# Kernel tuning notes

Measured on AMD Instinct MI355X. Metric: run time of the kernel, lower is better.

## Reference

```python
import jax, jax.numpy as jnp
import numpy as np

B_SZ, L, H, P = 16, 1024, 256, 256
DT_MIN, DT_MAX = 1e-3, 1e-1


def setup_inputs() -> dict:
    key = jax.random.key(0)
    ks = jax.random.split(key, 6)
    u = jax.random.normal(ks[0], (B_SZ, L, H), dtype=jnp.float32)
    # Stable diagonal init (stands in for HiPPO-LegS diag: negative real part,
    # spread imaginary parts) so exp(Lambda*Delta) has |.|<1 over long scans.
    Lambda_re = -0.5 * jnp.ones((P,), jnp.float32)
    Lambda_im = jnp.pi * jnp.arange(P, dtype=jnp.float32)
    Bp = jax.random.normal(ks[1], (P, H, 2), jnp.float32) / jnp.sqrt(2.0 * H)  # (P,H,2) real/imag
    Cp = jax.random.normal(ks[2], (H, P, 2), jnp.float32) / jnp.sqrt(2.0 * P)  # (H,P,2) real/imag
    D = jax.random.normal(ks[3], (H,), jnp.float32)
    log_step = (jax.random.uniform(ks[4], (P, 1), jnp.float32)
                * (jnp.log(DT_MAX) - jnp.log(DT_MIN)) + jnp.log(DT_MIN))
    return {"u": u, "Lambda_re": Lambda_re, "Lambda_im": Lambda_im,
            "B": Bp, "C": Cp, "D": D, "log_step": log_step}


def _binop(ei, ej):
    # S5 associative scan element: (A, Bu); compose linear recurrences.
    ai, bi = ei
    aj, bj = ej
    return aj * ai, aj * bi + bj


def reference(u, Lambda_re, Lambda_im, B, C, D, log_step):
    # clip_eigs=False, step_rescale=1.0, conj_sym=True, discretization='zoh'
    Lambda = Lambda_re + 1j * Lambda_im                     # (P,) complex
    B_tilde = B[..., 0] + 1j * B[..., 1]                    # (P,H) complex
    C_tilde = C[..., 0] + 1j * C[..., 1]                    # (H,P) complex
    Delta = jnp.exp(log_step[:, 0])                         # (P,)
    # ZOH discretization
    Lambda_bar = jnp.exp(Lambda * Delta)                    # (P,)
    B_bar = ((Lambda_bar - 1.0) / Lambda)[:, None] * B_tilde  # (P,H)
    # Input projection: (B, L, P) complex
    Bu = jnp.einsum('ph,blh->blp', B_bar, u.astype(B_bar.dtype))
    Lam = jnp.broadcast_to(Lambda_bar, Bu.shape)            # (B, L, P)
    # Parallel associative scan over time axis
    _, xs = jax.lax.associative_scan(_binop, (Lam, Bu), axis=1)  # states (B,L,P)
    # Output projection; conj_sym -> 2 * real part
    ys = 2.0 * jnp.einsum('hp,blp->blh', C_tilde, xs).real  # (B,L,H)
    return ys + D * u                                       # feedthrough
```

## Files before the change

### kernel.cpp

```cpp
#include <hip/hip_runtime.h>
#include <hip/hip_bf16.h>
#include <math.h>

#define BB     16
#define LSEQ   1024
#define HH     256
#define PP     256
#define MROWS  (BB*LSEQ)
#define LC     32
#define NC     (LSEQ/LC)
#define NCHUNK (BB*NC)

#define OFF_W1T  0u
#define OFF_W2T  262144u
#define OFF_PW   524288u
#define OFF_CEND 655360u
#define OFF_CARR 1703936u
#define OFF_XS   2752512u
#define OFF_UB   19529728u

typedef __attribute__((ext_vector_type(8))) short short8;
typedef __attribute__((ext_vector_type(4))) float floatx4;

__device__ __forceinline__ float bf2f(unsigned hs) {
    union { unsigned u; float f; } v; v.u = hs << 16; return v.f;
}
__device__ __forceinline__ unsigned short f2bs(float f) {
    __hip_bfloat16 h = __float2bfloat16(f);
    union { __hip_bfloat16 h; unsigned short s; } v; v.h = h; return v.s;
}
__device__ __forceinline__ unsigned packbf(float r, float i) {
    return (unsigned)f2bs(r) | ((unsigned)f2bs(i) << 16);
}
__device__ __forceinline__ void async16(const void* g, void* l) {
    __builtin_amdgcn_global_load_lds(
        (const __attribute__((address_space(1))) unsigned*)g,
        (__attribute__((address_space(3))) unsigned*)l, 16, 0, 0);
}
__device__ __forceinline__ float2 lam_pow(float lr, float li, float dtt) {
    float m = expf(lr * dtt);
    return make_float2(m * cosf(li * dtt), m * sinf(li * dtt));
}

__global__ void k_prep(const float* __restrict__ Bm, const float* __restrict__ Cm,
                       const float* __restrict__ Lr, const float* __restrict__ Li,
                       const float* __restrict__ ls, const float* __restrict__ u,
                       char* __restrict__ ws) {
    int blk = blockIdx.x, t = threadIdx.x;
    if (blk < 256) {
        int p = blk, h = t;
        float lr = Lr[p], li = Li[p];
        float dt = expf(ls[p]);
        float2 lam = lam_pow(lr, li, dt);
        float den = lr * lr + li * li;
        float nr = lam.x - 1.0f, ni = lam.y;
        float cr = (nr * lr + ni * li) / den;
        float ci = (ni * lr - nr * li) / den;
        float br = Bm[(p * HH + h) * 2 + 0];
        float bi = Bm[(p * HH + h) * 2 + 1];
        unsigned short* w1 = (unsigned short*)(ws + OFF_W1T);
        w1[(2 * p) * 256 + h]     = f2bs(cr * br - ci * bi);
        w1[(2 * p + 1) * 256 + h] = f2bs(cr * bi + ci * br);
        if (t <= 32)
            ((float2*)(ws + OFF_PW))[t * 256 + p] = lam_pow(lr, li, dt * (float)t);
    } else {
        int h = blk - 256, p = t;
        float c_r = Cm[(h * PP + p) * 2 + 0];
        float c_i = Cm[(h * PP + p) * 2 + 1];
        ((unsigned*)(ws + OFF_W2T))[h * 256 + p] = packbf(2.0f * c_r, -2.0f * c_i);
    }
    uint2* ub = (uint2*)(ws + OFF_UB);
    const float4* u4 = (const float4*)u;
    #pragma unroll
    for (int i = 0; i < 8; ++i) {
        size_t idx = (size_t)blk * 2048 + i * 256 + t;
        float4 v = u4[idx];
        ub[idx] = make_uint2(packbf(v.x, v.y), packbf(v.z, v.w));
    }
}

#define XSTR 140
__global__ __launch_bounds__(512, 2) void k_g1scan(
        const float* __restrict__ Lr, const float* __restrict__ Li,
        const float* __restrict__ ls, char* __restrict__ ws) {
    __shared__ char smem[36864];
    char* Asb = smem;
    char* Bsb = smem + 16384;
    unsigned short* X = (unsigned short*)smem;
    unsigned* X32 = (unsigned*)smem;
    const unsigned short* W1 = (const unsigned short*)(ws + OFF_W1T);
    const unsigned short* UB = (const unsigned short*)(ws + OFF_UB);
    const int tid = threadIdx.x, bx = blockIdx.x;
    const int ns = bx & 3, rg = bx >> 2;
    const int m0 = rg * 128, n0 = ns * 128;
    const int wave = tid >> 6, lane = tid & 63;
    const int q = lane >> 4, rr = lane & 15;
    const int c4 = lane & 3, r4 = lane >> 2;

    floatx4 acc[8];
    #pragma unroll
    for (int i = 0; i < 8; ++i) acc[i] = (floatx4)0.0f;

    for (int k0 = 0; k0 < 256; k0 += 64) {
        __syncthreads();
        #pragma unroll
        for (int t = 0; t < 2; ++t) {
            int idx = t * 8 + wave;
            int pan = idx & 1, rowg = idx >> 1;
            int row = rowg * 16 + r4;
            async16(UB + (size_t)(m0 + row) * 256 + k0 + pan * 32 + c4 * 8,
                    Asb + pan * 8192 + row * 64 + c4 * 16);
            async16(W1 + (size_t)(n0 + row) * 256 + k0 + pan * 32 + c4 * 8,
                    Bsb + pan * 8192 + row * 64 + c4 * 16);
        }
        __syncthreads();
        #pragma unroll
        for (int ks = 0; ks < 2; ++ks) {
            short8 b = *(const short8*)(Bsb + ks * 8192 + (wave * 16 + rr) * 64 + q * 16);
            #pragma unroll
            for (int i = 0; i < 8; ++i) {
                short8 a = *(const short8*)(Asb + ks * 8192 + (i * 16 + rr) * 64 + q * 16);
                acc[i] = __builtin_amdgcn_mfma_f32_16x16x32_bf16(a, b, acc[i], 0, 0, 0);
            }
        }
    }
    __syncthreads();
    #pragma unroll
    for (int i = 0; i < 8; ++i)
        #pragma unroll
        for (int r0 = 0; r0 < 4; ++r0)
            X[(i * 16 + q * 4 + r0) * XSTR + wave * 16 + rr] = f2bs(acc[i][r0]);
    __syncthreads();

    if (tid < 256) {
        const int ch = tid >> 6, pq = tid & 63;
        const int gp = (n0 >> 1) + pq;
        const float2 lam = lam_pow(Lr[gp], Li[gp], expf(ls[gp]));
        unsigned* xs32 = (unsigned*)(ws + OFF_XS);
        float xr = 0.0f, xi = 0.0f;
        for (int j = 0; j < LC; ++j) {
            unsigned cv = X32[(ch * 32 + j) * (XSTR / 2) + pq];
            float br = bf2f(cv & 0xffffu), bi = bf2f(cv >> 16);
            float nr = fmaf(lam.x, xr, fmaf(-lam.y, xi, br));
            float ni = fmaf(lam.x, xi, fmaf(lam.y, xr, bi));
            xr = nr; xi = ni;
            xs32[(size_t)(m0 + ch * 32 + j) * 256 + gp] = packbf(xr, xi);
        }
        ((float2*)(ws + OFF_CEND))[(size_t)(rg * 4 + ch) * 256 + gp] = make_float2(xr, xi);
    }
}

__global__ void k_carry(const float* __restrict__ Lr, const float* __restrict__ Li,
                        const float* __restrict__ ls, char* __restrict__ ws) {
    int p = threadIdx.x, b = blockIdx.x;
    float dt = expf(ls[p]);
    float2 g = lam_pow(Lr[p], Li[p], dt * (float)LC);
    const float2* cend = (const float2*)(ws + OFF_CEND);
    float2* carr = (float2*)(ws + OFF_CARR);
    float sr = 0.0f, si = 0.0f;
    for (int c = 0; c < NC; ++c) {
        size_t off = (size_t)(b * NC + c) * 256 + p;
        carr[off] = make_float2(sr, si);
        float2 e = cend[off];
        float nr = fmaf(g.x, sr, fmaf(-g.y, si, e.x));
        float ni = fmaf(g.x, si, fmaf(g.y, sr, e.y));
        sr = nr; si = ni;
    }
}

__global__ __launch_bounds__(256, 4) void k_gemm2fix(
        const char* __restrict__ ws_c, const float* __restrict__ D,
        const float* __restrict__ u, float* __restrict__ out) {
    __shared__ char Asb[8192];
    __shared__ char Bsb[16384];
    __shared__ float2 carrs[2][256];
    const unsigned short* W2 = (const unsigned short*)(ws_c + OFF_W2T);
    const unsigned* xs32 = (const unsigned*)(ws_c + OFF_XS);
    const float2* pw = (const float2*)(ws_c + OFF_PW);
    const float2* carr = (const float2*)(ws_c + OFF_CARR);

    const int tid = threadIdx.x;
    const int wave = tid >> 6, lane = tid & 63;
    const int q = lane >> 4, rr = lane & 15;
    const int c4 = lane & 3, r4 = lane >> 2;
    const int wm = wave & 1, wn = wave >> 1;
    const int m0 = blockIdx.y * 64, n0 = blockIdx.x * 128;

    {
        int cbase = m0 >> 5;
        carrs[0][tid] = carr[(size_t)cbase * 256 + tid];
        carrs[1][tid] = carr[(size_t)(cbase + 1) * 256 + tid];
    }

    floatx4 acc[2][4];
    #pragma unroll
    for (int i = 0; i < 2; ++i)
        #pragma unroll
        for (int j = 0; j < 4; ++j) acc[i][j] = (floatx4)0.0f;

    const int row = tid >> 2, qd = tid & 3;
    const int grow = m0 + row;
    const int jj = (grow & (LC - 1)) + 1;
    const int half = row >> 5;

    for (int k0 = 0; k0 < 512; k0 += 64) {
        __syncthreads();
        {
            int p0 = (k0 >> 1) + qd * 8;
            uint4 xa = *(const uint4*)(xs32 + (size_t)grow * 256 + p0);
            uint4 xb = *(const uint4*)(xs32 + (size_t)grow * 256 + p0 + 4);
            unsigned xv[8] = {xa.x, xa.y, xa.z, xa.w, xb.x, xb.y, xb.z, xb.w};
            const float2* pwp = pw + (size_t)jj * 256 + p0;
            const float2* cap = &carrs[half][p0];
            unsigned o[8];
            #pragma unroll
            for (int e = 0; e < 8; ++e) {
                float2 pwv = pwp[e];
                float2 cav = cap[e];
                float fr = pwv.x * cav.x - pwv.y * cav.y;
                float fi = pwv.x * cav.y + pwv.y * cav.x;
                o[e] = packbf(bf2f(xv[e] & 0xffffu) + fr, bf2f(xv[e] >> 16) + fi);
            }
            char* dst = Asb + (qd >> 1) * 4096 + row * 64 + (qd & 1) * 32;
            *(uint4*)dst        = make_uint4(o[0], o[1], o[2], o[3]);
            *(uint4*)(dst + 16) = make_uint4(o[4], o[5], o[6], o[7]);
        }
        #pragma unroll
        for (int t = 0; t < 4; ++t) {
            int idx = t * 4 + wave;
            int pan = idx & 1, rowg = idx >> 1;
            int rw = rowg * 16 + r4;
            async16(W2 + (size_t)(n0 + rw) * 512 + k0 + pan * 32 + c4 * 8,
                    Bsb + pan * 8192 + rw * 64 + c4 * 16);
        }
        __syncthreads();
        #pragma unroll
        for (int ks = 0; ks < 2; ++ks) {
            short8 a[2], bfr[4];
            #pragma unroll
            for (int i = 0; i < 2; ++i)
                a[i] = *(const short8*)(Asb + ks * 4096 +
                                        (wm * 32 + i * 16 + rr) * 64 + q * 16);
            #pragma unroll
            for (int j = 0; j < 4; ++j)
                bfr[j] = *(const short8*)(Bsb + ks * 8192 +
                                          ((wn * 64 + j * 16 + rr)) * 64 + q * 16);
            #pragma unroll
            for (int i = 0; i < 2; ++i)
                #pragma unroll
                for (int j = 0; j < 4; ++j)
                    acc[i][j] = __builtin_amdgcn_mfma_f32_16x16x32_bf16(a[i], bfr[j], acc[i][j], 0, 0, 0);
        }
    }

    #pragma unroll
    for (int i = 0; i < 2; ++i) {
        int mbase = m0 + wm * 32 + i * 16 + q * 4;
        #pragma unroll
        for (int j = 0; j < 4; ++j) {
            int col = n0 + wn * 64 + j * 16 + rr;
            #pragma unroll
            for (int r0 = 0; r0 < 4; ++r0) {
                int rw = mbase + r0;
                size_t gi = (size_t)rw * 256 + col;
                out[gi] = acc[i][j][r0] + D[col] * u[gi];
            }
        }
    }
}

extern "C" void kernel_launch(void* const* d_in, const int* in_sizes, int n_in,
                              void* d_out, int out_size, void* d_ws, size_t ws_size,
                              hipStream_t stream) {
    const float* u  = (const float*)d_in[0];
    const float* Lr = (const float*)d_in[1];
    const float* Li = (const float*)d_in[2];
    const float* Bm = (const float*)d_in[3];
    const float* Cm = (const float*)d_in[4];
    const float* D  = (const float*)d_in[5];
    const float* ls = (const float*)d_in[6];
    float* out = (float*)d_out;
    char* ws = (char*)d_ws;

    k_prep<<<512, 256, 0, stream>>>(Bm, Cm, Lr, Li, ls, u, ws);
    k_g1scan<<<512, 512, 0, stream>>>(Lr, Li, ls, ws);
    k_carry<<<BB, 256, 0, stream>>>(Lr, Li, ls, ws);
    k_gemm2fix<<<dim3(2, MROWS / 64), 256, 0, stream>>>(ws, D, u, out);
}
```

Baseline: 116.5 us.

## Fuse prep kernel into GEMM1 and carry kernels, converting inputs on the fly

Removes the separate prep kernel. GEMM1 now loads fp32 u and the raw B matrix straight from global memory, builds the discretized B_bar and converts both to bf16 while staging them into LDS. The C-weight packing and the Lambda power table move into the carry kernel. This saves one launch and the workspace round trip for the bf16 copy of u. In exchange GEMM1 uses synchronous register-staged loads instead of async global-to-LDS copies, and every block recomputes B_bar for its tile.

```diff
diff --git a/kernel.cpp b/kernel.cpp
--- a/kernel.cpp
+++ b/kernel.cpp
@@ -11,13 +11,11 @@
 #define NC     (LSEQ/LC)
 #define NCHUNK (BB*NC)
 
-#define OFF_W1T  0u
 #define OFF_W2T  262144u
 #define OFF_PW   524288u
 #define OFF_CEND 655360u
 #define OFF_CARR 1703936u
 #define OFF_XS   2752512u
-#define OFF_UB   19529728u
 
 typedef __attribute__((ext_vector_type(8))) short short8;
 typedef __attribute__((ext_vector_type(4))) float floatx4;
@@ -42,60 +40,35 @@
     return make_float2(m * cosf(li * dtt), m * sinf(li * dtt));
 }
 
-__global__ void k_prep(const float* __restrict__ Bm, const float* __restrict__ Cm,
-                       const float* __restrict__ Lr, const float* __restrict__ Li,
-                       const float* __restrict__ ls, const float* __restrict__ u,
-                       char* __restrict__ ws) {
-    int blk = blockIdx.x, t = threadIdx.x;
-    if (blk < 256) {
-        int p = blk, h = t;
-        float lr = Lr[p], li = Li[p];
-        float dt = expf(ls[p]);
-        float2 lam = lam_pow(lr, li, dt);
-        float den = lr * lr + li * li;
-        float nr = lam.x - 1.0f, ni = lam.y;
-        float cr = (nr * lr + ni * li) / den;
-        float ci = (ni * lr - nr * li) / den;
-        float br = Bm[(p * HH + h) * 2 + 0];
-        float bi = Bm[(p * HH + h) * 2 + 1];
-        unsigned short* w1 = (unsigned short*)(ws + OFF_W1T);
-        w1[(2 * p) * 256 + h]     = f2bs(cr * br - ci * bi);
-        w1[(2 * p + 1) * 256 + h] = f2bs(cr * bi + ci * br);
-        if (t <= 32)
-            ((float2*)(ws + OFF_PW))[t * 256 + p] = lam_pow(lr, li, dt * (float)t);
-    } else {
-        int h = blk - 256, p = t;
-        float c_r = Cm[(h * PP + p) * 2 + 0];
-        float c_i = Cm[(h * PP + p) * 2 + 1];
-        ((unsigned*)(ws + OFF_W2T))[h * 256 + p] = packbf(2.0f * c_r, -2.0f * c_i);
-    }
-    uint2* ub = (uint2*)(ws + OFF_UB);
-    const float4* u4 = (const float4*)u;
-    #pragma unroll
-    for (int i = 0; i < 8; ++i) {
-        size_t idx = (size_t)blk * 2048 + i * 256 + t;
-        float4 v = u4[idx];
-        ub[idx] = make_uint2(packbf(v.x, v.y), packbf(v.z, v.w));
-    }
-}
-
 #define XSTR 140
 __global__ __launch_bounds__(512, 2) void k_g1scan(
-        const float* __restrict__ Lr, const float* __restrict__ Li,
-        const float* __restrict__ ls, char* __restrict__ ws) {
-    __shared__ char smem[36864];
+        const float* __restrict__ u, const float* __restrict__ Lr,
+        const float* __restrict__ Li, const float* __restrict__ ls,
+        const float* __restrict__ Bm, char* __restrict__ ws) {
+    __shared__ char smem[35840];
     char* Asb = smem;
     char* Bsb = smem + 16384;
     unsigned short* X = (unsigned short*)smem;
     unsigned* X32 = (unsigned*)smem;
-    const unsigned short* W1 = (const unsigned short*)(ws + OFF_W1T);
-    const unsigned short* UB = (const unsigned short*)(ws + OFF_UB);
     const int tid = threadIdx.x, bx = blockIdx.x;
     const int ns = bx & 3, rg = bx >> 2;
     const int m0 = rg * 128, n0 = ns * 128;
     const int wave = tid >> 6, lane = tid & 63;
     const int q = lane >> 4, rr = lane & 15;
-    const int c4 = lane & 3, r4 = lane >> 2;
+
+    const int pl = tid >> 3, oct = tid & 7;
+    const int gpb = (n0 >> 1) + pl;
+    float crc, cic;
+    {
+        float lr = Lr[gpb], li = Li[gpb];
+        float dt = expf(ls[gpb]);
+        float2 lam = lam_pow(lr, li, dt);
+        float den = lr * lr + li * li;
+        float nr = lam.x - 1.0f, ni = lam.y;
+        crc = (nr * lr + ni * li) / den;
+        cic = (ni * lr - nr * li) / den;
+    }
+    const int arow = tid >> 2, koff = (tid & 3) * 16;
 
     floatx4 acc[8];
     #pragma unroll
@@ -103,15 +76,34 @@
 
     for (int k0 = 0; k0 < 256; k0 += 64) {
         __syncthreads();
-        #pragma unroll
-        for (int t = 0; t < 2; ++t) {
-            int idx = t * 8 + wave;
-            int pan = idx & 1, rowg = idx >> 1;
-            int row = rowg * 16 + r4;
-            async16(UB + (size_t)(m0 + row) * 256 + k0 + pan * 32 + c4 * 8,
-                    Asb + pan * 8192 + row * 64 + c4 * 16);
-            async16(W1 + (size_t)(n0 + row) * 256 + k0 + pan * 32 + c4 * 8,
-                    Bsb + pan * 8192 + row * 64 + c4 * 16);
+        {
+            const float4* up = (const float4*)(u + (size_t)(m0 + arow) * 256 + k0 + koff);
+            float4 v0 = up[0], v1 = up[1], v2 = up[2], v3 = up[3];
+            char* dst = Asb + (koff >> 5) * 8192 + arow * 64 + (koff & 31) * 2;
+            *(uint4*)dst = make_uint4(packbf(v0.x, v0.y), packbf(v0.z, v0.w),
+                                      packbf(v1.x, v1.y), packbf(v1.z, v1.w));
+            *(uint4*)(dst + 16) = make_uint4(packbf(v2.x, v2.y), packbf(v2.z, v2.w),
+                                             packbf(v3.x, v3.y), packbf(v3.z, v3.w));
+        }
+        {
+            const float4* bp = (const float4*)(Bm + ((size_t)gpb * 256 + k0 + oct * 8) * 2);
+            float4 b0 = bp[0], b1 = bp[1], b2 = bp[2], b3 = bp[3];
+            float re[8], im[8];
+            re[0]=crc*b0.x-cic*b0.y; im[0]=crc*b0.y+cic*b0.x;
+            re[1]=crc*b0.z-cic*b0.w; im[1]=crc*b0.w+cic*b0.z;
+            re[2]=crc*b1.x-cic*b1.y; im[2]=crc*b1.y+cic*b1.x;
+            re[3]=crc*b1.z-cic*b1.w; im[3]=crc*b1.w+cic*b1.z;
+            re[4]=crc*b2.x-cic*b2.y; im[4]=crc*b2.y+cic*b2.x;
+            re[5]=crc*b2.z-cic*b2.w; im[5]=crc*b2.w+cic*b2.z;
+            re[6]=crc*b3.x-cic*b3.y; im[6]=crc*b3.y+cic*b3.x;
+            re[7]=crc*b3.z-cic*b3.w; im[7]=crc*b3.w+cic*b3.z;
+            int pan = oct >> 2, hh = (oct & 3) * 8;
+            char* dr = Bsb + pan * 8192 + (2 * pl) * 64 + hh * 2;
+            char* di = Bsb + pan * 8192 + (2 * pl + 1) * 64 + hh * 2;
+            *(uint4*)dr = make_uint4(packbf(re[0], re[1]), packbf(re[2], re[3]),
+                                     packbf(re[4], re[5]), packbf(re[6], re[7]));
+            *(uint4*)di = make_uint4(packbf(im[0], im[1]), packbf(im[2], im[3]),
+                                     packbf(im[4], im[5]), packbf(im[6], im[7]));
         }
         __syncthreads();
         #pragma unroll
@@ -151,10 +143,34 @@
 }
 
 __global__ void k_carry(const float* __restrict__ Lr, const float* __restrict__ Li,
-                        const float* __restrict__ ls, char* __restrict__ ws) {
-    int p = threadIdx.x, b = blockIdx.x;
-    float dt = expf(ls[p]);
-    float2 g = lam_pow(Lr[p], Li[p], dt * (float)LC);
+                        const float* __restrict__ ls, const float* __restrict__ Cm,
+                        char* __restrict__ ws) {
+    const int tid = threadIdx.x, b = blockIdx.x;
+
+    {
+        int h = b * 16 + (tid >> 4);
+        int p0 = (tid & 15) * 16;
+        unsigned* w2 = (unsigned*)(ws + OFF_W2T);
+        const float2* cp = (const float2*)Cm + (size_t)h * 256 + p0;
+        #pragma unroll
+        for (int e = 0; e < 16; ++e) {
+            float2 c = cp[e];
+            w2[(size_t)h * 256 + p0 + e] = packbf(2.0f * c.x, -2.0f * c.y);
+        }
+    }
+
+    const int p = tid;
+    const float lr = Lr[p], li = Li[p];
+    const float dt = expf(ls[p]);
+
+    {
+        float2* pw = (float2*)(ws + OFF_PW);
+        pw[(2 * b) * 256 + p]     = lam_pow(lr, li, dt * (float)(2 * b));
+        pw[(2 * b + 1) * 256 + p] = lam_pow(lr, li, dt * (float)(2 * b + 1));
+        if (b == 0) pw[32 * 256 + p] = lam_pow(lr, li, dt * 32.0f);
+    }
+
+    float2 g = lam_pow(lr, li, dt * (float)LC);
     const float2* cend = (const float2*)(ws + OFF_CEND);
     float2* carr = (float2*)(ws + OFF_CARR);
     float sr = 0.0f, si = 0.0f;
@@ -282,8 +298,7 @@
     float* out = (float*)d_out;
     char* ws = (char*)d_ws;
 
-    k_prep<<<512, 256, 0, stream>>>(Bm, Cm, Lr, Li, ls, u, ws);
-    k_g1scan<<<512, 512, 0, stream>>>(Lr, Li, ls, ws);
-    k_carry<<<BB, 256, 0, stream>>>(Lr, Li, ls, ws);
+    k_g1scan<<<512, 512, 0, stream>>>(u, Lr, Li, ls, Bm, ws);
+    k_carry<<<BB, 256, 0, stream>>>(Lr, Li, ls, Cm, ws);
     k_gemm2fix<<<dim3(2, MROWS / 64), 256, 0, stream>>>(ws, D, u, out);
 }
```

After: 121.8 us. 1.05x slower.
